# Kernel tuning notes

Measured on AMD Instinct MI355X. Metric: run time of the kernel, lower is better.

## Reference

```python
import jax, jax.numpy as jnp
import numpy as np

THRESHOLD = 0.5
EPS = 1e-8


def cos_sim(a, b):
    # a: [M, D], b: [N, D] -> [M, N] cosine similarity
    a_n = jnp.linalg.norm(a, axis=1, keepdims=True)
    b_n = jnp.linalg.norm(b, axis=1, keepdims=True)
    a_norm = a / jnp.maximum(a_n, EPS)
    b_norm = b / jnp.maximum(b_n, EPS)
    return a_norm @ b_norm.T


def setup_inputs() -> dict:
    key = jax.random.key(0)
    k1, k2, k3, k4 = jax.random.split(key, 4)
    N1, N2, FEA_FT, W_FT = 8192, 8192, 128, 64
    fea1 = jax.random.normal(k1, (N1, FEA_FT), dtype=jnp.float32)
    fea2 = jax.random.normal(k2, (N2, FEA_FT), dtype=jnp.float32)
    # xavier_uniform with relu gain sqrt(2): limit = gain * sqrt(6/(fan_in+fan_out))
    gain = float(np.sqrt(2.0))
    limit = gain * float(np.sqrt(6.0 / (FEA_FT + W_FT)))
    w1 = jax.random.uniform(k3, (FEA_FT, W_FT), minval=-limit, maxval=limit, dtype=jnp.float32)
    w2 = jax.random.uniform(k4, (FEA_FT, W_FT), minval=-limit, maxval=limit, dtype=jnp.float32)
    return {"fea1": fea1, "fea2": fea2, "w1": w1, "w2": w2}


def reference(fea1, fea2, w1, w2):
    embed1 = fea1 @ w1  # [N1, w_ft]
    embed2 = fea2 @ w2  # [N2, w_ft]
    sim_up = cos_sim(embed1, embed2)  # [N1, N2]
    sims_up = jnp.where(sim_up < THRESHOLD, jnp.zeros_like(sim_up), sim_up)
    sim_uu = cos_sim(embed1, embed1)  # [N1, N1]
    sims_uu = jnp.where(sim_uu < THRESHOLD, jnp.zeros_like(sim_uu), sim_uu)
    # Edge lists in the original are nonzero(sims_up)/nonzero(sims_uu); we return
    # the thresholded similarity matrices (jit-safe, fixed shape), stacked.
    return jnp.stack([sims_up, sims_uu], axis=0)  # [2, N, N]
```

## Files before the change

### kernel.cpp

```cpp
#include <hip/hip_runtime.h>

#define THRESH 0.5f

constexpr int N  = 8192;
constexpr int FD = 128;
constexpr int WD = 64;

__global__ __launch_bounds__(256) void embed_norm(
    const float* __restrict__ fea1, const float* __restrict__ fea2,
    const float* __restrict__ w1,   const float* __restrict__ w2,
    float* __restrict__ E1n, float* __restrict__ E2n) {
  const int which = blockIdx.y;
  const float* __restrict__ fea = which ? fea2 : fea1;
  const float* __restrict__ w   = which ? w2   : w1;
  float* __restrict__ En        = which ? E2n  : E1n;

  __shared__ float wl[FD * WD];
  __shared__ float fl[32][FD];

  const int t    = threadIdx.x;
  const int row0 = blockIdx.x * 32;

#pragma unroll
  for (int i = 0; i < 8; ++i) {
    const int idx = (t + i * 256) * 4;
    *(float4*)&wl[idx] = *(const float4*)&w[idx];
  }
#pragma unroll
  for (int i = 0; i < 4; ++i) {
    const int idx = t + i * 256;
    const int r = idx >> 5;
    const int c = (idx & 31) * 4;
    *(float4*)&fl[r][c] = *(const float4*)&fea[(size_t)(row0 + r) * FD + c];
  }
  __syncthreads();

  const int wave = t >> 6, lane = t & 63;
#pragma unroll 1
  for (int rr = 0; rr < 8; ++rr) {
    const int r = wave * 8 + rr;
    float acc = 0.f;
#pragma unroll 16
    for (int k = 0; k < FD; ++k)
      acc = fmaf(fl[r][k], wl[k * WD + lane], acc);
    float ss = acc * acc;
#pragma unroll
    for (int m = 32; m >= 1; m >>= 1) ss += __shfl_xor(ss, m, 64);
    const float scale = 1.f / fmaxf(sqrtf(ss), 1e-8f);
    En[(size_t)(row0 + r) * WD + lane] = acc * scale;
  }
}

__global__ __launch_bounds__(256, 2) void sim_kernel(
    const float* __restrict__ E1, const float* __restrict__ E2,
    float* __restrict__ out) {
  __shared__ float Asm[WD][128];
  __shared__ float Bsm[WD][128];

  const int bi = blockIdx.y, bj = blockIdx.x;
  const int t  = threadIdx.x;
  const int tx = t & 15, ty = t >> 4;

  float* __restrict__ out0 = out;
  float* __restrict__ out1 = out + (size_t)N * N;

  auto stage = [&](float sm[WD][128], const float* __restrict__ src) {
#pragma unroll
    for (int i = 0; i < 8; ++i) {
      const int idx = t + i * 256;
      const int m = idx & 127, kq = idx >> 7;
      float4 v = *(const float4*)&src[m * WD + kq * 4];
      sm[kq * 4 + 0][m] = v.x;
      sm[kq * 4 + 1][m] = v.y;
      sm[kq * 4 + 2][m] = v.z;
      sm[kq * 4 + 3][m] = v.w;
    }
  };

  auto thr = [](float v) { return v < THRESH ? 0.f : v; };

  float acc[8][8];

  auto compute = [&]() {
#pragma unroll
    for (int r = 0; r < 8; ++r)
#pragma unroll
      for (int c = 0; c < 8; ++c) acc[r][c] = 0.f;
#pragma unroll 2
    for (int k = 0; k < WD; ++k) {
      const float4 a0 = *(const float4*)&Asm[k][ty * 4];
      const float4 a1 = *(const float4*)&Asm[k][64 + ty * 4];
      const float4 b0 = *(const float4*)&Bsm[k][tx * 4];
      const float4 b1 = *(const float4*)&Bsm[k][64 + tx * 4];
      const float av[8] = {a0.x, a0.y, a0.z, a0.w, a1.x, a1.y, a1.z, a1.w};
      const float bv[8] = {b0.x, b0.y, b0.z, b0.w, b1.x, b1.y, b1.z, b1.w};
#pragma unroll
      for (int r = 0; r < 8; ++r)
#pragma unroll
        for (int c = 0; c < 8; ++c)
          acc[r][c] = fmaf(av[r], bv[c], acc[r][c]);
    }
  };

  auto write_direct = [&](float* __restrict__ dst) {
#pragma unroll
    for (int r = 0; r < 8; ++r) {
      const int R = (r < 4) ? (ty * 4 + r) : (64 + ty * 4 + (r - 4));
      float* p = dst + (size_t)(bi * 128 + R) * N + bj * 128;
      float4 v0 = make_float4(thr(acc[r][0]), thr(acc[r][1]), thr(acc[r][2]), thr(acc[r][3]));
      float4 v1 = make_float4(thr(acc[r][4]), thr(acc[r][5]), thr(acc[r][6]), thr(acc[r][7]));
      *(float4*)(p + tx * 4)      = v0;
      *(float4*)(p + 64 + tx * 4) = v1;
    }
  };

  stage(Asm, E1 + (size_t)bi * 128 * WD);
  stage(Bsm, E2 + (size_t)bj * 128 * WD);
  __syncthreads();
  compute();
  write_direct(out0);

  if (bi <= bj) {
    __syncthreads();
    stage(Bsm, E1 + (size_t)bj * 128 * WD);
    __syncthreads();
    compute();
    write_direct(out1);

    if (bi < bj) {
#pragma unroll
      for (int c = 0; c < 8; ++c) {
        const int C = (c < 4) ? (tx * 4 + c) : (64 + tx * 4 + (c - 4));
        float* p = out1 + (size_t)(bj * 128 + C) * N + bi * 128;
        float4 v0 = make_float4(thr(acc[0][c]), thr(acc[1][c]), thr(acc[2][c]), thr(acc[3][c]));
        float4 v1 = make_float4(thr(acc[4][c]), thr(acc[5][c]), thr(acc[6][c]), thr(acc[7][c]));
        *(float4*)(p + ty * 4)      = v0;
        *(float4*)(p + 64 + ty * 4) = v1;
      }
    }
  }
}

extern "C" void kernel_launch(void* const* d_in, const int* in_sizes, int n_in,
                              void* d_out, int out_size, void* d_ws, size_t ws_size,
                              hipStream_t stream) {
  const float* fea1 = (const float*)d_in[0];
  const float* fea2 = (const float*)d_in[1];
  const float* w1   = (const float*)d_in[2];
  const float* w2   = (const float*)d_in[3];
  float* out = (float*)d_out;

  float* E1n = (float*)d_ws;
  float* E2n = E1n + (size_t)N * WD;

  embed_norm<<<dim3(N / 32, 2), 256, 0, stream>>>(fea1, fea2, w1, w2, E1n, E2n);
  sim_kernel<<<dim3(64, 64), 256, 0, stream>>>(E1n, E2n, out);
}
```

Measured before the change: 640.4 us.

## Compute similarities with split-bf16 MFMA and fp32 fixup near threshold

Replaces the fp32 FMA tiled similarity kernel with a matrix-core kernel. Each normalized embedding is split into high and low bf16 parts, and four bf16 MFMA products approximate fp32 accuracy. Entries within a small band of the threshold are appended to a fix list through a global atomic, and a third kernel recomputes them in fp32. The new kernel also drops the symmetric-reuse trick for the uu plane and reads operands straight from global memory without LDS staging. This trades extra MFMA work, atomics and an extra launch for much higher matrix throughput, while the kernel is likely still bound by the 512MB output write.

After: 641.9 us. No clear change (+0.2%).

```diff
diff --git a/kernel.cpp b/kernel.cpp
--- a/kernel.cpp
+++ b/kernel.cpp
@@ -1,19 +1,41 @@
 #include <hip/hip_runtime.h>
 
 #define THRESH 0.5f
+#define BAND   1e-3f
 
 constexpr int N  = 8192;
 constexpr int FD = 128;
 constexpr int WD = 64;
+constexpr unsigned FIX_CAP = 16u << 20;
+
+typedef __attribute__((ext_vector_type(8)))  short short8;
+typedef __attribute__((ext_vector_type(4)))  float f32x4;
+
+static __device__ __forceinline__ unsigned short f2bf(float x) {
+  union { float f; unsigned u; } v; v.f = x;
+  unsigned r = v.u + 0x7FFFu + ((v.u >> 16) & 1u);
+  return (unsigned short)(r >> 16);
+}
+static __device__ __forceinline__ float bf2f(unsigned short h) {
+  union { unsigned u; float f; } v; v.u = (unsigned)h << 16;
+  return v.f;
+}
 
 __global__ __launch_bounds__(256) void embed_norm(
     const float* __restrict__ fea1, const float* __restrict__ fea2,
     const float* __restrict__ w1,   const float* __restrict__ w2,
-    float* __restrict__ E1n, float* __restrict__ E2n) {
+    float* __restrict__ E1n, float* __restrict__ E2n,
+    unsigned short* __restrict__ E1h, unsigned short* __restrict__ E1l,
+    unsigned short* __restrict__ E2h, unsigned short* __restrict__ E2l,
+    unsigned* __restrict__ fix_cnt) {
+  if (blockIdx.x == 0 && blockIdx.y == 0 && threadIdx.x == 0) *fix_cnt = 0;
+
   const int which = blockIdx.y;
   const float* __restrict__ fea = which ? fea2 : fea1;
   const float* __restrict__ w   = which ? w2   : w1;
-  float* __restrict__ En        = which ? E2n  : E1n;
+  float*          En = which ? E2n : E1n;
+  unsigned short* Eh = which ? E2h : E1h;
+  unsigned short* El = which ? E2l : E1l;
 
   __shared__ float wl[FD * WD];
   __shared__ float fl[32][FD];
@@ -47,97 +69,96 @@
 #pragma unroll
     for (int m = 32; m >= 1; m >>= 1) ss += __shfl_xor(ss, m, 64);
     const float scale = 1.f / fmaxf(sqrtf(ss), 1e-8f);
-    En[(size_t)(row0 + r) * WD + lane] = acc * scale;
+    const float e = acc * scale;
+    const size_t o = (size_t)(row0 + r) * WD + lane;
+    En[o] = e;
+    const unsigned short h = f2bf(e);
+    Eh[o] = h;
+    El[o] = f2bf(e - bf2f(h));
   }
 }
 
-__global__ __launch_bounds__(256, 2) void sim_kernel(
+__global__ __launch_bounds__(256) void sim_mfma(
+    const unsigned short* __restrict__ E1h, const unsigned short* __restrict__ E1l,
+    const unsigned short* __restrict__ E2h, const unsigned short* __restrict__ E2l,
+    float* __restrict__ out,
+    unsigned* __restrict__ fix_cnt, unsigned* __restrict__ fix_lst) {
+  const int bi = blockIdx.y, bj = blockIdx.x;
+  const int t = threadIdx.x, w = t >> 6, lane = t & 63;
+  const int wr = w >> 1, wc = w & 1;
+  const int row0 = bi * 128 + wr * 64;
+  const int col0 = bj * 128 + wc * 64;
+  const int fr = lane & 15;
+  const int fg = lane >> 4;
+
+#pragma unroll 1
+  for (int plane = 0; plane < 2; ++plane) {
+    const unsigned short* __restrict__ Bh = plane ? E1h : E2h;
+    const unsigned short* __restrict__ Bl = plane ? E1l : E2l;
+
+    f32x4 acc[4][4] = {};
+#pragma unroll
+    for (int ks = 0; ks < 2; ++ks) {
+      const int koff = ks * 32 + fg * 8;
+      short8 ah[4], al[4], bh[4], bl[4];
+#pragma unroll
+      for (int ti = 0; ti < 4; ++ti) {
+        const size_t ra = (size_t)(row0 + ti * 16 + fr) * WD + koff;
+        ah[ti] = *(const short8*)(E1h + ra);
+        al[ti] = *(const short8*)(E1l + ra);
+        const size_t rb = (size_t)(col0 + ti * 16 + fr) * WD + koff;
+        bh[ti] = *(const short8*)(Bh + rb);
+        bl[ti] = *(const short8*)(Bl + rb);
+      }
+#pragma unroll
+      for (int ti = 0; ti < 4; ++ti)
+#pragma unroll
+        for (int tj = 0; tj < 4; ++tj) {
+          acc[ti][tj] = __builtin_amdgcn_mfma_f32_16x16x32_bf16(ah[ti], bh[tj], acc[ti][tj], 0, 0, 0);
+          acc[ti][tj] = __builtin_amdgcn_mfma_f32_16x16x32_bf16(ah[ti], bl[tj], acc[ti][tj], 0, 0, 0);
+          acc[ti][tj] = __builtin_amdgcn_mfma_f32_16x16x32_bf16(al[ti], bh[tj], acc[ti][tj], 0, 0, 0);
+          acc[ti][tj] = __builtin_amdgcn_mfma_f32_16x16x32_bf16(al[ti], bl[tj], acc[ti][tj], 0, 0, 0);
+        }
+    }
+
+    float* __restrict__ o = out + (size_t)plane * N * N;
+#pragma unroll
+    for (int ti = 0; ti < 4; ++ti)
+#pragma unroll
+      for (int tj = 0; tj < 4; ++tj)
+#pragma unroll
+        for (int r = 0; r < 4; ++r) {
+          const int R = row0 + ti * 16 + fg * 4 + r;
+          const int C = col0 + tj * 16 + fr;
+          const float v = acc[ti][tj][r];
+          if (fabsf(v - THRESH) < BAND) {
+            const unsigned idx = atomicAdd(fix_cnt, 1u);
+            if (idx < FIX_CAP)
+              fix_lst[idx] = ((unsigned)plane << 26) | ((unsigned)R << 13) | (unsigned)C;
+          }
+          o[(size_t)R * N + C] = (v < THRESH) ? 0.f : v;
+        }
+  }
+}
+
+__global__ __launch_bounds__(256) void fixup(
     const float* __restrict__ E1, const float* __restrict__ E2,
-    float* __restrict__ out) {
-  __shared__ float Asm[WD][128];
-  __shared__ float Bsm[WD][128];
-
-  const int bi = blockIdx.y, bj = blockIdx.x;
-  const int t  = threadIdx.x;
-  const int tx = t & 15, ty = t >> 4;
-
-  float* __restrict__ out0 = out;
-  float* __restrict__ out1 = out + (size_t)N * N;
-
-  auto stage = [&](float sm[WD][128], const float* __restrict__ src) {
-#pragma unroll
-    for (int i = 0; i < 8; ++i) {
-      const int idx = t + i * 256;
-      const int m = idx & 127, kq = idx >> 7;
-      float4 v = *(const float4*)&src[m * WD + kq * 4];
-      sm[kq * 4 + 0][m] = v.x;
-      sm[kq * 4 + 1][m] = v.y;
-      sm[kq * 4 + 2][m] = v.z;
-      sm[kq * 4 + 3][m] = v.w;
-    }
-  };
-
-  auto thr = [](float v) { return v < THRESH ? 0.f : v; };
-
-  float acc[8][8];
-
-  auto compute = [&]() {
-#pragma unroll
-    for (int r = 0; r < 8; ++r)
-#pragma unroll
-      for (int c = 0; c < 8; ++c) acc[r][c] = 0.f;
-#pragma unroll 2
-    for (int k = 0; k < WD; ++k) {
-      const float4 a0 = *(const float4*)&Asm[k][ty * 4];
-      const float4 a1 = *(const float4*)&Asm[k][64 + ty * 4];
-      const float4 b0 = *(const float4*)&Bsm[k][tx * 4];
-      const float4 b1 = *(const float4*)&Bsm[k][64 + tx * 4];
-      const float av[8] = {a0.x, a0.y, a0.z, a0.w, a1.x, a1.y, a1.z, a1.w};
-      const float bv[8] = {b0.x, b0.y, b0.z, b0.w, b1.x, b1.y, b1.z, b1.w};
-#pragma unroll
-      for (int r = 0; r < 8; ++r)
-#pragma unroll
-        for (int c = 0; c < 8; ++c)
-          acc[r][c] = fmaf(av[r], bv[c], acc[r][c]);
-    }
-  };
-
-  auto write_direct = [&](float* __restrict__ dst) {
-#pragma unroll
-    for (int r = 0; r < 8; ++r) {
-      const int R = (r < 4) ? (ty * 4 + r) : (64 + ty * 4 + (r - 4));
-      float* p = dst + (size_t)(bi * 128 + R) * N + bj * 128;
-      float4 v0 = make_float4(thr(acc[r][0]), thr(acc[r][1]), thr(acc[r][2]), thr(acc[r][3]));
-      float4 v1 = make_float4(thr(acc[r][4]), thr(acc[r][5]), thr(acc[r][6]), thr(acc[r][7]));
-      *(float4*)(p + tx * 4)      = v0;
-      *(float4*)(p + 64 + tx * 4) = v1;
-    }
-  };
-
-  stage(Asm, E1 + (size_t)bi * 128 * WD);
-  stage(Bsm, E2 + (size_t)bj * 128 * WD);
-  __syncthreads();
-  compute();
-  write_direct(out0);
-
-  if (bi <= bj) {
-    __syncthreads();
-    stage(Bsm, E1 + (size_t)bj * 128 * WD);
-    __syncthreads();
-    compute();
-    write_direct(out1);
-
-    if (bi < bj) {
-#pragma unroll
-      for (int c = 0; c < 8; ++c) {
-        const int C = (c < 4) ? (tx * 4 + c) : (64 + tx * 4 + (c - 4));
-        float* p = out1 + (size_t)(bj * 128 + C) * N + bi * 128;
-        float4 v0 = make_float4(thr(acc[0][c]), thr(acc[1][c]), thr(acc[2][c]), thr(acc[3][c]));
-        float4 v1 = make_float4(thr(acc[4][c]), thr(acc[5][c]), thr(acc[6][c]), thr(acc[7][c]));
-        *(float4*)(p + ty * 4)      = v0;
-        *(float4*)(p + 64 + ty * 4) = v1;
-      }
-    }
+    float* __restrict__ out,
+    const unsigned* __restrict__ fix_cnt, const unsigned* __restrict__ fix_lst) {
+  unsigned n = *fix_cnt;
+  if (n > FIX_CAP) n = FIX_CAP;
+  for (unsigned idx = blockIdx.x * blockDim.x + threadIdx.x; idx < n;
+       idx += gridDim.x * blockDim.x) {
+    const unsigned e = fix_lst[idx];
+    const int plane = (int)(e >> 26);
+    const int i = (int)((e >> 13) & 8191);
+    const int j = (int)(e & 8191);
+    const float* __restrict__ B = plane ? E1 : E2;
+    float s = 0.f;
+#pragma unroll 16
+    for (int k = 0; k < WD; ++k)
+      s = fmaf(E1[i * WD + k], B[j * WD + k], s);
+    out[(size_t)plane * N * N + (size_t)i * N + j] = (s < THRESH) ? 0.f : s;
   }
 }
 
@@ -150,9 +171,19 @@
   const float* w2   = (const float*)d_in[3];
   float* out = (float*)d_out;
 
-  float* E1n = (float*)d_ws;
-  float* E2n = E1n + (size_t)N * WD;
+  char* ws = (char*)d_ws;
+  float*          E1n = (float*)(ws);
+  float*          E2n = (float*)(ws + (2u << 20));
+  unsigned short* E1h = (unsigned short*)(ws + (4u << 20));
+  unsigned short* E1l = (unsigned short*)(ws + (5u << 20));
+  unsigned short* E2h = (unsigned short*)(ws + (6u << 20));
+  unsigned short* E2l = (unsigned short*)(ws + (7u << 20));
+  unsigned*   fix_cnt = (unsigned*)(ws + (8u << 20));
+  unsigned*   fix_lst = (unsigned*)(ws + (8u << 20) + 256);
 
-  embed_norm<<<dim3(N / 32, 2), 256, 0, stream>>>(fea1, fea2, w1, w2, E1n, E2n);
-  sim_kernel<<<dim3(64, 64), 256, 0, stream>>>(E1n, E2n, out);
+  embed_norm<<<dim3(N / 32, 2), 256, 0, stream>>>(
+      fea1, fea2, w1, w2, E1n, E2n, E1h, E1l, E2h, E2l, fix_cnt);
+  sim_mfma<<<dim3(64, 64), 256, 0, stream>>>(
+      E1h, E1l, E2h, E2l, out, fix_cnt, fix_lst);
+  fixup<<<64, 256, 0, stream>>>(E1n, E2n, out, fix_cnt, fix_lst);
 }
```
